# Optimization experiments

Hardware: AMD Instinct MI355X
Metric: run time of the kernel (lower is better)

Reference implementation:

```python
import jax, jax.numpy as jnp
import numpy as np

N_NODES = 50000
N_EDGES = 800000
NFEAT = 128
NHID = 64  # gc1: NFEAT -> 2*NHID, gc2: 2*NHID -> NHID


def setup_inputs() -> dict:
    key = jax.random.key(0)
    k1, k2, k3, k4, k5 = jax.random.split(key, 5)
    feat = jax.random.normal(k1, (N_NODES, NFEAT), dtype=jnp.float32)
    src = jax.random.randint(k2, (N_EDGES,), 0, N_NODES, dtype=jnp.int32)
    dst = jax.random.randint(k3, (N_EDGES,), 0, N_NODES, dtype=jnp.int32)
    # GraphConv weights: (in_feats, out_feats), xavier-like scale
    W1 = jax.random.normal(k4, (NFEAT, 2 * NHID), dtype=jnp.float32) / np.sqrt(NFEAT)
    b1 = jnp.zeros((2 * NHID,), dtype=jnp.float32)
    W2 = jax.random.normal(k5, (2 * NHID, NHID), dtype=jnp.float32) / np.sqrt(2 * NHID)
    b2 = jnp.zeros((NHID,), dtype=jnp.float32)
    return {"feat": feat, "src": src, "dst": dst, "W1": W1, "b1": b1, "W2": W2, "b2": b2}


def _graph_conv(feat, src, dst, W, b):
    """DGL GraphConv, norm='both', allow_zero_in_degree=True.
    h = D_in^{-1/2} A (D_out^{-1/2} x) W + b, with degrees clamped to >= 1.
    Applies W before aggregation when in_feats > out_feats (saves bandwidth)."""
    N = feat.shape[0]
    ones = jnp.ones(src.shape[0], dtype=feat.dtype)
    deg_out = jnp.clip(jax.ops.segment_sum(ones, src, num_segments=N), 1.0)
    deg_in = jnp.clip(jax.ops.segment_sum(ones, dst, num_segments=N), 1.0)
    h = feat * (deg_out ** -0.5)[:, None]
    mult_first = W.shape[0] > W.shape[1]
    if mult_first:
        h = h @ W
    agg = jax.ops.segment_sum(h[src], dst, num_segments=N)  # [N, d]
    if not mult_first:
        agg = agg @ W
    return agg * (deg_in ** -0.5)[:, None] + b


def reference(feat, src, dst, W1, b1, W2, b2):
    x = jax.nn.relu(_graph_conv(feat, src, dst, W1, b1))
    # dropout is inactive in eval mode (F.dropout training=False)
    x = _graph_conv(x, src, dst, W2, b2)
    return jax.nn.log_softmax(x, axis=1)
```

## Files before the change

### kernel.cpp

```cpp
#include <hip/hip_runtime.h>
#include <math.h>


constexpr int NF   = 128;
constexpr int NH   = 64;
constexpr int CAP  = 48;
constexpr int EPB  = 4096;
constexpr int BCAP = 8192;
constexpr int NBKMAX = 256;

typedef unsigned int uint;
typedef unsigned short ushort_t;
typedef __attribute__((ext_vector_type(8))) short short8;
typedef __attribute__((ext_vector_type(4))) float f32x4;

__device__ __forceinline__ float bflo(uint u) { return __uint_as_float(u << 16); }
__device__ __forceinline__ float bfhi(uint u) { return __uint_as_float(u & 0xffff0000u); }
__device__ __forceinline__ uint packbf(float a, float b) {
    uint ua = __float_as_uint(a), ub = __float_as_uint(b);
    uint ra = (ua + 0x7fffu + ((ua >> 16) & 1u)) >> 16;
    uint rb = (ub + 0x7fffu + ((ub >> 16) & 1u)) >> 16;
    return ra | (rb << 16);
}
__device__ __forceinline__ ushort_t bf16u(float f) {
    uint u = __float_as_uint(f);
    return (ushort_t)((u + 0x7fffu + ((u >> 16) & 1u)) >> 16);
}
__device__ __forceinline__ short8 as_short8(uint4 u) {
    union { uint4 u; short8 s; } x; x.u = u; return x.s;
}

__global__ __launch_bounds__(1024) void partition_kernel(
        const int* __restrict__ src, const int* __restrict__ dst,
        uint* __restrict__ pairs_g, ushort_t* __restrict__ srcb_g,
        int* __restrict__ dcur, int* __restrict__ scur,
        const float* __restrict__ W1, const float* __restrict__ W2,
        uint* __restrict__ W1p, uint* __restrict__ W2p,
        int E, int nbk, int nchunk) {
    if (blockIdx.x >= nchunk) {
        int i = (blockIdx.x - nchunk) * 1024 + threadIdx.x;
        if (i < 8192) {
            int jp = i & 3, g = (i >> 2) & 3, n = (i >> 4) & 127, kk = i >> 11;
            int k = kk * 32 + g * 8 + jp * 2;
            W1p[i] = packbf(W1[k * 128 + n], W1[(k + 1) * 128 + n]);
        } else if (i < 12288) {
            int j = i - 8192;
            int jp = j & 3, g = (j >> 2) & 3, n = (j >> 4) & 63, kk = j >> 10;
            int k = kk * 32 + g * 8 + jp * 2;
            W2p[j] = packbf(W2[k * 64 + n], W2[(k + 1) * 64 + n]);
        }
        return;
    }
    __shared__ uint     pl[EPB];
    __shared__ ushort_t sl[EPB];
    __shared__ int dh[NBKMAX], sh[NBKMAX];
    __shared__ int doff[NBKMAX], soff[NBKMAX];
    __shared__ int dbase[NBKMAX], sbase[NBKMAX];
    __shared__ int dpos[NBKMAX], spos[NBKMAX];
    int tid = threadIdx.x;
    int e0 = blockIdx.x * EPB;
    int ecnt = min(EPB, E - e0);

    for (int b = tid; b < nbk; b += 1024) { dh[b] = 0; sh[b] = 0; }
    __syncthreads();
    for (int i = tid; i < ecnt; i += 1024) {
        atomicAdd(&dh[dst[e0 + i] >> 8], 1);
        atomicAdd(&sh[src[e0 + i] >> 8], 1);
    }
    __syncthreads();
    if (tid == 0)  { int run = 0; for (int b = 0; b < nbk; ++b) { doff[b] = run; run += dh[b]; } }
    if (tid == 64) { int run = 0; for (int b = 0; b < nbk; ++b) { soff[b] = run; run += sh[b]; } }
    for (int b = tid; b < nbk; b += 1024) {
        dbase[b] = atomicAdd(&dcur[b], dh[b]);
        sbase[b] = atomicAdd(&scur[b], sh[b]);
    }
    __syncthreads();
    for (int b = tid; b < nbk; b += 1024) { dpos[b] = doff[b]; spos[b] = soff[b]; }
    __syncthreads();
    for (int i = tid; i < ecnt; i += 1024) {
        int s = src[e0 + i], d = dst[e0 + i];
        int p = atomicAdd(&dpos[d >> 8], 1);
        pl[p] = ((uint)s << 16) | (uint)d;
        int q = atomicAdd(&spos[s >> 8], 1);
        sl[q] = (ushort_t)s;
    }
    __syncthreads();
    for (int i = tid; i < ecnt; i += 1024) {
        uint e = pl[i];
        int b = (int)((e & 0xffffu) >> 8);
        int gp = dbase[b] + (i - doff[b]);
        if (gp < BCAP) pairs_g[(size_t)b * BCAP + gp] = e;
        ushort_t sv = sl[i];
        int b2 = (int)(sv >> 8);
        int gq = sbase[b2] + (i - soff[b2]);
        if (gq < BCAP) srcb_g[(size_t)b2 * BCAP + gq] = sv;
    }
}

__global__ __launch_bounds__(1024) void bin_kernel(
        const uint* __restrict__ pairs_g, const ushort_t* __restrict__ srcb_g,
        const int* __restrict__ dcur, const int* __restrict__ scur,
        const float* __restrict__ feat, uint* __restrict__ featb,
        ushort_t* __restrict__ slots, int* __restrict__ lens,
        float* __restrict__ s_in, float* __restrict__ s_out, int N) {
    __shared__ ushort_t slots_l[256 * CAP];
    __shared__ int cin[256], cout[256];
    __shared__ float souts[256];
    int tid = threadIdx.x;
    int b = blockIdx.x;
    int lo = b << 8;
    for (int r = tid; r < 256; r += 1024) { cin[r] = 0; cout[r] = 0; }
    __syncthreads();
    int dn = min(dcur[b], BCAP);
    for (int i = tid; i < dn; i += 1024) {
        uint e = pairs_g[(size_t)b * BCAP + i];
        int r = (int)(e & 255u);
        int p = atomicAdd(&cin[r], 1);
        if (p < CAP) slots_l[r * CAP + p] = (ushort_t)(e >> 16);
    }
    int sn = min(scur[b], BCAP);
    for (int i = tid; i < sn; i += 1024)
        atomicAdd(&cout[(int)srcb_g[(size_t)b * BCAP + i] - lo], 1);
    __syncthreads();
    int nrow = min(256, N - lo);
    {
        const uint4* sl4 = (const uint4*)slots_l;
        uint4* gs4 = (uint4*)(slots + (size_t)lo * CAP);
        int lim4 = nrow * (CAP / 8);
        for (int k = tid; k < 256 * CAP / 8; k += 1024)
            if (k < lim4) gs4[k] = sl4[k];
    }
    for (int r = tid; r < nrow; r += 1024) {
        int node = lo + r;
        int ci = cin[r];
        lens[node]  = min(ci, CAP);
        s_in[node]  = rsqrtf((float)max(ci, 1));
        float so    = rsqrtf((float)max(cout[r], 1));
        s_out[node] = so;
        souts[r]    = so;
    }
    __syncthreads();
    for (int k = tid; k < nrow * 16; k += 1024) {
        int r = k >> 4, ch = k & 15;
        float sc = souts[r];
        const float4* f4 = (const float4*)(feat + (size_t)(lo + r) * NF + ch * 8);
        float4 a = f4[0], c = f4[1];
        uint4 o;
        o.x = packbf(a.x * sc, a.y * sc);
        o.y = packbf(a.z * sc, a.w * sc);
        o.z = packbf(c.x * sc, c.y * sc);
        o.w = packbf(c.z * sc, c.w * sc);
        *(uint4*)(featb + (size_t)(lo + r) * 64 + ch * 4) = o;
    }
}

__global__ __launch_bounds__(256) void agg1_kernel(const uint* __restrict__ featb,
        const int* __restrict__ lens, const ushort_t* __restrict__ slots,
        uint* __restrict__ agg1b, int N) {
    int wave = threadIdx.x >> 6;
    int lane = threadIdx.x & 63;
    int q   = lane >> 4;
    int sub = lane & 15;
    int node = blockIdx.x * 4 + wave;
    if (node >= N) return;
    int beg = node * CAP;
    int len = lens[node];
    float acc[8] = {0.f, 0.f, 0.f, 0.f, 0.f, 0.f, 0.f, 0.f};
    if (len > 0) {
        int li = min(lane, len - 1);
        int sidx = (int)slots[beg + li];
        int quads = (len + 3) >> 2;
        #pragma unroll 4
        for (int k = 0; k < quads; ++k) {
            int e = 4 * k + q;
            int s = __shfl(sidx, e, 64);
            if (e < len) {
                uint4 v = *(const uint4*)(featb + (size_t)s * 64 + sub * 4);
                acc[0] += bflo(v.x); acc[1] += bfhi(v.x);
                acc[2] += bflo(v.y); acc[3] += bfhi(v.y);
                acc[4] += bflo(v.z); acc[5] += bfhi(v.z);
                acc[6] += bflo(v.w); acc[7] += bfhi(v.w);
            }
        }
    }
    #pragma unroll
    for (int j = 0; j < 8; ++j) {
        acc[j] += __shfl_xor(acc[j], 32, 64);
        acc[j] += __shfl_xor(acc[j], 16, 64);
    }
    if (q == 0) {
        uint4 o;
        o.x = packbf(acc[0], acc[1]);
        o.y = packbf(acc[2], acc[3]);
        o.z = packbf(acc[4], acc[5]);
        o.w = packbf(acc[6], acc[7]);
        *(uint4*)(agg1b + (size_t)node * 64 + sub * 4) = o;
    }
}

__global__ __launch_bounds__(256) void fused_gemm_kernel(
        const uint* __restrict__ agg1b, const uint* __restrict__ W1p,
        const float* __restrict__ b1, const uint* __restrict__ W2p,
        const float* __restrict__ s_in, const float* __restrict__ s_out,
        uint* __restrict__ h2b, int N) {
    __shared__ ushort_t x1t[64][136];
    __shared__ float sin_l[64], sout_l[64];
    int t = threadIdx.x;
    int base = blockIdx.x * 64;
    int w    = t >> 6;
    int lane = t & 63;
    int c = lane & 15;
    int g = lane >> 4;

    if (t < 64)       sin_l[t]        = (base + t < N) ? s_in[base + t] : 0.f;
    else if (t < 128) sout_l[t - 64]  = (base + t - 64 < N) ? s_out[base + t - 64] : 0.f;
    __syncthreads();

    f32x4 zero = {0.f, 0.f, 0.f, 0.f};
    f32x4 c1[4][2];
    #pragma unroll
    for (int mt = 0; mt < 4; ++mt) { c1[mt][0] = zero; c1[mt][1] = zero; }
    #pragma unroll
    for (int kk = 0; kk < 4; ++kk) {
        short8 bf[2];
        #pragma unroll
        for (int ntl = 0; ntl < 2; ++ntl) {
            int n = (2 * w + ntl) * 16 + c;
            bf[ntl] = as_short8(*(const uint4*)(W1p + (size_t)kk * 2048 + n * 16 + g * 4));
        }
        #pragma unroll
        for (int mt = 0; mt < 4; ++mt) {
            int row = base + mt * 16 + c;
            short8 af = as_short8(*(const uint4*)(agg1b + (size_t)row * 64 + kk * 16 + g * 4));
            c1[mt][0] = __builtin_amdgcn_mfma_f32_16x16x32_bf16(af, bf[0], c1[mt][0], 0, 0, 0);
            c1[mt][1] = __builtin_amdgcn_mfma_f32_16x16x32_bf16(af, bf[1], c1[mt][1], 0, 0, 0);
        }
    }
    float bias0 = b1[(2 * w) * 16 + c];
    float bias1 = b1[(2 * w + 1) * 16 + c];
    #pragma unroll
    for (int mt = 0; mt < 4; ++mt) {
        #pragma unroll
        for (int r = 0; r < 4; ++r) {
            int rl = mt * 16 + g * 4 + r;
            float si = sin_l[rl], so = sout_l[rl];
            x1t[rl][(2 * w) * 16 + c]     = bf16u(fmaxf(fmaf(si, c1[mt][0][r], bias0), 0.f) * so);
            x1t[rl][(2 * w + 1) * 16 + c] = bf16u(fmaxf(fmaf(si, c1[mt][1][r], bias1), 0.f) * so);
        }
    }
    __syncthreads();

    f32x4 c2[4];
    #pragma unroll
    for (int mt = 0; mt < 4; ++mt) c2[mt] = zero;
    #pragma unroll
    for (int kk = 0; kk < 4; ++kk) {
        int n = w * 16 + c;
        short8 bf2 = as_short8(*(const uint4*)(W2p + (size_t)kk * 1024 + n * 16 + g * 4));
        #pragma unroll
        for (int mt = 0; mt < 4; ++mt) {
            short8 af = *(const short8*)&x1t[mt * 16 + c][kk * 32 + g * 8];
            c2[mt] = __builtin_amdgcn_mfma_f32_16x16x32_bf16(af, bf2, c2[mt], 0, 0, 0);
        }
    }
    __syncthreads();

    ushort_t* h2t = &x1t[0][0];
    #pragma unroll
    for (int mt = 0; mt < 4; ++mt) {
        #pragma unroll
        for (int r = 0; r < 4; ++r) {
            int rl = mt * 16 + g * 4 + r;
            h2t[rl * 72 + w * 16 + c] = bf16u(c2[mt][r]);
        }
    }
    __syncthreads();
    int row = t >> 2, ch = t & 3;
    if (base + row < N) {
        uint4 v0 = *(const uint4*)(h2t + row * 72 + ch * 16);
        uint4 v1 = *(const uint4*)(h2t + row * 72 + ch * 16 + 8);
        *(uint4*)(h2b + (size_t)(base + row) * 32 + ch * 8)     = v0;
        *(uint4*)(h2b + (size_t)(base + row) * 32 + ch * 8 + 4) = v1;
    }
}

__global__ __launch_bounds__(256) void agg2_softmax_kernel(const uint* __restrict__ h2b,
        const int* __restrict__ lens, const ushort_t* __restrict__ slots,
        const float* __restrict__ s_in, const float* __restrict__ b2,
        float* __restrict__ out, int N) {
    int wave = threadIdx.x >> 6;
    int lane = threadIdx.x & 63;
    int oct = lane >> 3;
    int sub = lane & 7;
    int node = blockIdx.x * 4 + wave;
    if (node >= N) return;
    int beg = node * CAP;
    int len = lens[node];
    float acc[8] = {0.f, 0.f, 0.f, 0.f, 0.f, 0.f, 0.f, 0.f};
    if (len > 0) {
        int li = min(lane, len - 1);
        int sidx = (int)slots[beg + li];
        int octs = (len + 7) >> 3;
        #pragma unroll 4
        for (int k = 0; k < octs; ++k) {
            int e = 8 * k + oct;
            int s = __shfl(sidx, e, 64);
            if (e < len) {
                uint4 v = *(const uint4*)(h2b + (size_t)s * 32 + sub * 4);
                acc[0] += bflo(v.x); acc[1] += bfhi(v.x);
                acc[2] += bflo(v.y); acc[3] += bfhi(v.y);
                acc[4] += bflo(v.z); acc[5] += bfhi(v.z);
                acc[6] += bflo(v.w); acc[7] += bfhi(v.w);
            }
        }
    }
    #pragma unroll
    for (int j = 0; j < 8; ++j) {
        acc[j] += __shfl_xor(acc[j], 32, 64);
        acc[j] += __shfl_xor(acc[j], 16, 64);
        acc[j] += __shfl_xor(acc[j], 8, 64);
    }
    float si = s_in[node];
    float4 bb0 = *(const float4*)(b2 + sub * 8);
    float4 bb1 = *(const float4*)(b2 + sub * 8 + 4);
    float v[8];
    v[0] = fmaf(acc[0], si, bb0.x); v[1] = fmaf(acc[1], si, bb0.y);
    v[2] = fmaf(acc[2], si, bb0.z); v[3] = fmaf(acc[3], si, bb0.w);
    v[4] = fmaf(acc[4], si, bb1.x); v[5] = fmaf(acc[5], si, bb1.y);
    v[6] = fmaf(acc[6], si, bb1.z); v[7] = fmaf(acc[7], si, bb1.w);

    float m = v[0];
    #pragma unroll
    for (int j = 1; j < 8; ++j) m = fmaxf(m, v[j]);
    m = fmaxf(m, __shfl_xor(m, 4, 64));
    m = fmaxf(m, __shfl_xor(m, 2, 64));
    m = fmaxf(m, __shfl_xor(m, 1, 64));
    float s8 = 0.f;
    #pragma unroll
    for (int j = 0; j < 8; ++j) s8 += expf(v[j] - m);
    s8 += __shfl_xor(s8, 4, 64);
    s8 += __shfl_xor(s8, 2, 64);
    s8 += __shfl_xor(s8, 1, 64);
    float ls = m + logf(s8);
    if (oct == 0) {
        float4 o0 = make_float4(v[0] - ls, v[1] - ls, v[2] - ls, v[3] - ls);
        float4 o1 = make_float4(v[4] - ls, v[5] - ls, v[6] - ls, v[7] - ls);
        *(float4*)(out + (size_t)node * NH + sub * 8)     = o0;
        *(float4*)(out + (size_t)node * NH + sub * 8 + 4) = o1;
    }
}

extern "C" void kernel_launch(void* const* d_in, const int* in_sizes, int n_in,
                              void* d_out, int out_size, void* d_ws, size_t ws_size,
                              hipStream_t stream) {
    const float* feat = (const float*)d_in[0];
    const int*   src  = (const int*)d_in[1];
    const int*   dst  = (const int*)d_in[2];
    const float* W1   = (const float*)d_in[3];
    const float* b1   = (const float*)d_in[4];
    const float* W2   = (const float*)d_in[5];
    const float* b2   = (const float*)d_in[6];
    float* out = (float*)d_out;

    int N = in_sizes[0] / NF;
    int E = in_sizes[1];
    int nbk = (N + 255) >> 8;
    int nchunk = (E + EPB - 1) / EPB;
    int Npad = (N + 63) & ~63;

    char* p = (char*)d_ws;
    auto alloc = [&](size_t bytes) -> char* {
        char* q = p;
        p += (bytes + 255) & ~(size_t)255;
        return q;
    };
    int*      dcur  = (int*)alloc((size_t)nbk * 4);
    int*      scur  = (int*)alloc((size_t)nbk * 4);
    uint*     pairs = (uint*)alloc((size_t)nbk * BCAP * 4);
    ushort_t* srcb  = (ushort_t*)alloc((size_t)nbk * BCAP * 2);
    ushort_t* slots = (ushort_t*)alloc((size_t)N * CAP * 2);
    int*      lens  = (int*)alloc((size_t)N * 4);
    float*    s_out = (float*)alloc((size_t)N * 4);
    float*    s_in  = (float*)alloc((size_t)N * 4);
    uint*     featb = (uint*)alloc((size_t)N * 64 * 4);
    uint*     agg1b = (uint*)alloc((size_t)Npad * 64 * 4);
    uint*     W1p   = (uint*)alloc(8192 * 4);
    uint*     W2p   = (uint*)alloc(4096 * 4);
    uint*     h2b   = (uint*)alloc((size_t)N * 32 * 4);

    size_t cur_span = (size_t)((char*)scur - (char*)dcur) + (size_t)nbk * 4;
    hipMemsetAsync(dcur, 0, cur_span, stream);

    partition_kernel<<<nchunk + 12, 1024, 0, stream>>>(
        src, dst, pairs, srcb, dcur, scur, W1, W2, W1p, W2p, E, nbk, nchunk);
    bin_kernel<<<nbk, 1024, 0, stream>>>(pairs, srcb, dcur, scur, feat, featb,
                                         slots, lens, s_in, s_out, N);
    agg1_kernel<<<(N + 3) / 4, 256, 0, stream>>>(featb, lens, slots, agg1b, N);
    fused_gemm_kernel<<<(N + 63) / 64, 256, 0, stream>>>(agg1b, W1p, b1, W2p, s_in, s_out, h2b, N);
    agg2_softmax_kernel<<<(N + 3) / 4, 256, 0, stream>>>(h2b, lens, slots, s_in, b2, out, N);
}
```

Measured before the change: 174.5 us.

## Count out-degrees with global atomics instead of binning source ids

Out-degree is now counted by per-edge global atomic adds into a per-node array, which removes the second bucketed partition of source ids, its shared-memory staging, its global scatter, and the matching histogram pass in the bin kernel. The serial single-thread prefix scan over buckets is replaced by a wave-level shuffle scan. The cost is 800k global atomics spread over 50k addresses and a larger memset, in exchange for less shared-memory traffic and fewer global writes and reads.

```diff
diff --git a/kernel.cpp b/kernel.cpp
--- a/kernel.cpp
+++ b/kernel.cpp
@@ -32,8 +32,8 @@
 
 __global__ __launch_bounds__(1024) void partition_kernel(
         const int* __restrict__ src, const int* __restrict__ dst,
-        uint* __restrict__ pairs_g, ushort_t* __restrict__ srcb_g,
-        int* __restrict__ dcur, int* __restrict__ scur,
+        uint* __restrict__ pairs_g, int* __restrict__ deg_out,
+        int* __restrict__ dcur,
         const float* __restrict__ W1, const float* __restrict__ W2,
         uint* __restrict__ W1p, uint* __restrict__ W2p,
         int E, int nbk, int nchunk) {
@@ -51,38 +51,47 @@
         }
         return;
     }
-    __shared__ uint     pl[EPB];
-    __shared__ ushort_t sl[EPB];
-    __shared__ int dh[NBKMAX], sh[NBKMAX];
-    __shared__ int doff[NBKMAX], soff[NBKMAX];
-    __shared__ int dbase[NBKMAX], sbase[NBKMAX];
-    __shared__ int dpos[NBKMAX], spos[NBKMAX];
+    __shared__ uint pl[EPB];
+    __shared__ int dh[NBKMAX], doff[NBKMAX];
+    __shared__ int dbase[NBKMAX], dpos[NBKMAX];
     int tid = threadIdx.x;
     int e0 = blockIdx.x * EPB;
     int ecnt = min(EPB, E - e0);
 
-    for (int b = tid; b < nbk; b += 1024) { dh[b] = 0; sh[b] = 0; }
+    for (int b = tid; b < nbk; b += 1024) dh[b] = 0;
     __syncthreads();
     for (int i = tid; i < ecnt; i += 1024) {
         atomicAdd(&dh[dst[e0 + i] >> 8], 1);
-        atomicAdd(&sh[src[e0 + i] >> 8], 1);
-    }
-    __syncthreads();
-    if (tid == 0)  { int run = 0; for (int b = 0; b < nbk; ++b) { doff[b] = run; run += dh[b]; } }
-    if (tid == 64) { int run = 0; for (int b = 0; b < nbk; ++b) { soff[b] = run; run += sh[b]; } }
-    for (int b = tid; b < nbk; b += 1024) {
-        dbase[b] = atomicAdd(&dcur[b], dh[b]);
-        sbase[b] = atomicAdd(&scur[b], sh[b]);
-    }
-    __syncthreads();
-    for (int b = tid; b < nbk; b += 1024) { dpos[b] = doff[b]; spos[b] = soff[b]; }
+        atomicAdd(&deg_out[src[e0 + i]], 1);
+    }
+    __syncthreads();
+    if (tid < 64) {
+        int l = tid, b0 = l * 4;
+        int v0 = (b0     < nbk) ? dh[b0]     : 0;
+        int v1 = (b0 + 1 < nbk) ? dh[b0 + 1] : 0;
+        int v2 = (b0 + 2 < nbk) ? dh[b0 + 2] : 0;
+        int v3 = (b0 + 3 < nbk) ? dh[b0 + 3] : 0;
+        int lsum = v0 + v1 + v2 + v3;
+        int sc = lsum;
+        #pragma unroll
+        for (int off = 1; off < 64; off <<= 1) {
+            int t = __shfl_up(sc, off, 64);
+            if (l >= off) sc += t;
+        }
+        int excl = sc - lsum;
+        if (b0     < nbk) doff[b0]     = excl;
+        if (b0 + 1 < nbk) doff[b0 + 1] = excl + v0;
+        if (b0 + 2 < nbk) doff[b0 + 2] = excl + v0 + v1;
+        if (b0 + 3 < nbk) doff[b0 + 3] = excl + v0 + v1 + v2;
+    }
+    for (int b = tid; b < nbk; b += 1024) dbase[b] = atomicAdd(&dcur[b], dh[b]);
+    __syncthreads();
+    for (int b = tid; b < nbk; b += 1024) dpos[b] = doff[b];
     __syncthreads();
     for (int i = tid; i < ecnt; i += 1024) {
         int s = src[e0 + i], d = dst[e0 + i];
         int p = atomicAdd(&dpos[d >> 8], 1);
         pl[p] = ((uint)s << 16) | (uint)d;
-        int q = atomicAdd(&spos[s >> 8], 1);
-        sl[q] = (ushort_t)s;
     }
     __syncthreads();
     for (int i = tid; i < ecnt; i += 1024) {
@@ -90,26 +99,22 @@
         int b = (int)((e & 0xffffu) >> 8);
         int gp = dbase[b] + (i - doff[b]);
         if (gp < BCAP) pairs_g[(size_t)b * BCAP + gp] = e;
-        ushort_t sv = sl[i];
-        int b2 = (int)(sv >> 8);
-        int gq = sbase[b2] + (i - soff[b2]);
-        if (gq < BCAP) srcb_g[(size_t)b2 * BCAP + gq] = sv;
     }
 }
 
 __global__ __launch_bounds__(1024) void bin_kernel(
-        const uint* __restrict__ pairs_g, const ushort_t* __restrict__ srcb_g,
-        const int* __restrict__ dcur, const int* __restrict__ scur,
+        const uint* __restrict__ pairs_g, const int* __restrict__ dcur,
+        const int* __restrict__ deg_out,
         const float* __restrict__ feat, uint* __restrict__ featb,
         ushort_t* __restrict__ slots, int* __restrict__ lens,
         float* __restrict__ s_in, float* __restrict__ s_out, int N) {
     __shared__ ushort_t slots_l[256 * CAP];
-    __shared__ int cin[256], cout[256];
+    __shared__ int cin[256];
     __shared__ float souts[256];
     int tid = threadIdx.x;
     int b = blockIdx.x;
     int lo = b << 8;
-    for (int r = tid; r < 256; r += 1024) { cin[r] = 0; cout[r] = 0; }
+    for (int r = tid; r < 256; r += 1024) cin[r] = 0;
     __syncthreads();
     int dn = min(dcur[b], BCAP);
     for (int i = tid; i < dn; i += 1024) {
@@ -118,9 +123,6 @@
         int p = atomicAdd(&cin[r], 1);
         if (p < CAP) slots_l[r * CAP + p] = (ushort_t)(e >> 16);
     }
-    int sn = min(scur[b], BCAP);
-    for (int i = tid; i < sn; i += 1024)
-        atomicAdd(&cout[(int)srcb_g[(size_t)b * BCAP + i] - lo], 1);
     __syncthreads();
     int nrow = min(256, N - lo);
     {
@@ -135,7 +137,7 @@
         int ci = cin[r];
         lens[node]  = min(ci, CAP);
         s_in[node]  = rsqrtf((float)max(ci, 1));
-        float so    = rsqrtf((float)max(cout[r], 1));
+        float so    = rsqrtf((float)max(deg_out[node], 1));
         s_out[node] = so;
         souts[r]    = so;
     }
@@ -375,9 +377,8 @@
         return q;
     };
     int*      dcur  = (int*)alloc((size_t)nbk * 4);
-    int*      scur  = (int*)alloc((size_t)nbk * 4);
+    int*      dego  = (int*)alloc((size_t)N * 4);
     uint*     pairs = (uint*)alloc((size_t)nbk * BCAP * 4);
-    ushort_t* srcb  = (ushort_t*)alloc((size_t)nbk * BCAP * 2);
     ushort_t* slots = (ushort_t*)alloc((size_t)N * CAP * 2);
     int*      lens  = (int*)alloc((size_t)N * 4);
     float*    s_out = (float*)alloc((size_t)N * 4);
@@ -388,12 +389,12 @@
     uint*     W2p   = (uint*)alloc(4096 * 4);
     uint*     h2b   = (uint*)alloc((size_t)N * 32 * 4);
 
-    size_t cur_span = (size_t)((char*)scur - (char*)dcur) + (size_t)nbk * 4;
-    hipMemsetAsync(dcur, 0, cur_span, stream);
+    size_t zero_span = (size_t)((char*)dego - (char*)dcur) + (size_t)N * 4;
+    hipMemsetAsync(dcur, 0, zero_span, stream);
 
     partition_kernel<<<nchunk + 12, 1024, 0, stream>>>(
-        src, dst, pairs, srcb, dcur, scur, W1, W2, W1p, W2p, E, nbk, nchunk);
-    bin_kernel<<<nbk, 1024, 0, stream>>>(pairs, srcb, dcur, scur, feat, featb,
+        src, dst, pairs, dego, dcur, W1, W2, W1p, W2p, E, nbk, nchunk);
+    bin_kernel<<<nbk, 1024, 0, stream>>>(pairs, dcur, dego, feat, featb,
                                          slots, lens, s_in, s_out, N);
     agg1_kernel<<<(N + 3) / 4, 256, 0, stream>>>(featb, lens, slots, agg1b, N);
     fused_gemm_kernel<<<(N + 63) / 64, 256, 0, stream>>>(agg1b, W1p, b1, W2p, s_in, s_out, h2b, N);
```

Result: slower. 203.0 us (+16.4%).
